# Optimization experiments

Measured on AMD Instinct MI355X. Metric: run time of the kernel, lower is better.

## Reference

```python
import jax, jax.numpy as jnp
import numpy as np

# Problem constants (would come from parameter_group in the original module)
N_POS = 512      # number of scan positions
BATCH = 32       # diffraction patterns per batch
N_OPR = 4        # OPR (orthogonal probe relaxation) modes
N_MODES = 8      # incoherent probe modes
H_OBJ = W_OBJ = 1024
HP = WP = 256    # probe / patch size
N_SLICES = 4     # multislice object
WAVELENGTH = 1.24e-10   # m (10 keV X-rays)
PIXEL = 1.0e-8          # m object pixel size
DZ = 2.0e-6             # m slice spacing


def _as_complex(x):
    return jax.lax.complex(x[..., 0], x[..., 1])


def _angular_spectrum_tf():
    # Transfer function H(fx,fy) = exp(i*dz*kz), kz = 2*pi/lambda * sqrt(1-(l*fx)^2-(l*fy)^2)
    fy = np.fft.fftfreq(HP, d=PIXEL)
    fx = np.fft.fftfreq(WP, d=PIXEL)
    FY, FX = np.meshgrid(fy, fx, indexing='ij')
    arg = 1.0 - (WAVELENGTH * FX) ** 2 - (WAVELENGTH * FY) ** 2
    kz = 2.0 * np.pi / WAVELENGTH * np.sqrt(np.maximum(arg, 0.0))
    tf = np.exp(1j * DZ * kz) * (arg > 0)  # evanescent cutoff
    return jnp.asarray(tf, jnp.complex64)

_TF = _angular_spectrum_tf()


def setup_inputs() -> dict:
    key = jax.random.key(0)
    k1, k2, k3, k4, k5 = jax.random.split(key, 5)
    object_ri = jax.random.normal(k1, (N_SLICES, H_OBJ, W_OBJ, 2), jnp.float32) * 0.1
    # make object roughly a weak phase/amplitude modulator around 1
    object_ri = object_ri.at[..., 0].add(1.0)
    probe_ri = jax.random.normal(k2, (N_OPR, N_MODES, HP, WP, 2), jnp.float32)
    opr_weights = jax.random.normal(k3, (N_POS, N_OPR), jnp.float32) * 0.1
    opr_weights = opr_weights.at[:, 0].add(1.0)
    # positions (row, col) such that the 256x256 patch fits inside the object
    positions = jax.random.uniform(k4, (N_POS, 2), jnp.float32,
                                   minval=16.0, maxval=float(H_OBJ - HP - 16))
    indices = jax.random.randint(k5, (BATCH,), 0, N_POS, jnp.int32)
    return {"object_ri": object_ri, "probe_ri": probe_ri,
            "opr_weights": opr_weights, "positions": positions, "indices": indices}


def reference(object_ri, probe_ri, opr_weights, positions, indices):
    obj = _as_complex(object_ri)      # (S, H, W)
    probe = _as_complex(probe_ri)     # (K, M, h, w)
    pos = positions[indices]          # (B, 2)
    rpos = jnp.round(pos)
    frac = pos - rpos                 # fractional shifts compensated on probe
    ipos = rpos.astype(jnp.int32)

    # --- gather object patches at rounded positions: (B, S, h, w) ---
    def get_patch(rc):
        return jax.lax.dynamic_slice(obj, (0, rc[0], rc[1]), (N_SLICES, HP, WP))
    patches = jax.vmap(get_patch)(ipos)

    # --- unique probes via OPR weighting of mode 0 ---
    w = opr_weights[indices].astype(probe.dtype)           # (B, K)
    p0 = jnp.einsum('bk,khw->bhw', w, probe[:, 0])         # (B, h, w)
    pk = jnp.broadcast_to(probe[0, 1:], (pos.shape[0], N_MODES - 1, HP, WP))
    uprobe = jnp.concatenate([p0[:, None], pk], axis=1)    # (B, M, h, w)

    # --- subpixel Fourier shift of probes by fractional positions ---
    fy = jnp.fft.fftfreq(HP).astype(jnp.float32)
    fx = jnp.fft.fftfreq(WP).astype(jnp.float32)
    ramp = frac[:, 0, None, None] * fy[:, None] + frac[:, 1, None, None] * fx[None, :]
    phase = jnp.exp(jax.lax.complex(jnp.zeros_like(ramp), -2.0 * jnp.pi * ramp))  # (B, h, w)
    uprobe = jnp.fft.ifft2(jnp.fft.fft2(uprobe) * phase[:, None])

    # --- multislice propagation through the object ---
    psi = uprobe
    for s in range(N_SLICES):
        psi = patches[:, s, None] * psi                    # modulate
        if s < N_SLICES - 1:
            psi = jnp.fft.ifft2(jnp.fft.fft2(psi) * _TF)   # angular spectrum

    # --- far-field (Fourier) propagation to detector ---
    psi_far = jnp.fft.fftshift(
        jnp.fft.fft2(jnp.fft.ifftshift(psi, axes=(-2, -1)), norm='ortho'),
        axes=(-2, -1))
    # incoherent sum over probe modes -> detector intensities (B, h, w)
    return jnp.sum(jnp.abs(psi_far) ** 2, axis=1)
```

## Files before the change

### kernel.cpp

```cpp
#include <hip/hip_runtime.h>
#include <math.h>

#define HP 256
#define NB 32
#define NM 8
#define NK 4
#define NS 4
#define HOBJ 1024

__device__ __forceinline__ float2 cmul(float2 a, float2 b) {
    return make_float2(fmaf(a.x, b.x, -a.y * b.y), fmaf(a.x, b.y, a.y * b.x));
}

__constant__ float COS16[10] = {1.f, 0.9238795325f, 0.7071067812f, 0.3826834324f, 0.f,
                                -0.3826834324f, -0.7071067812f, -0.9238795325f, -1.f, -0.9238795325f};
__constant__ float SIN16[10] = {0.f, 0.3826834324f, 0.7071067812f, 0.9238795325f, 1.f,
                                0.9238795325f, 0.7071067812f, 0.3826834324f, 0.f, -0.3826834324f};

template <int S>
__device__ __forceinline__ void dft4(float2 a, float2 b, float2 c, float2 d,
                                     float2* o0, float2* o1, float2* o2, float2* o3) {
    float2 apc = make_float2(a.x + c.x, a.y + c.y);
    float2 amc = make_float2(a.x - c.x, a.y - c.y);
    float2 bpd = make_float2(b.x + d.x, b.y + d.y);
    float2 bmd = make_float2(b.x - d.x, b.y - d.y);
    float2 ib = (S < 0) ? make_float2(bmd.y, -bmd.x) : make_float2(-bmd.y, bmd.x);
    *o0 = make_float2(apc.x + bpd.x, apc.y + bpd.y);
    *o1 = make_float2(amc.x + ib.x, amc.y + ib.y);
    *o2 = make_float2(apc.x - bpd.x, apc.y - bpd.y);
    *o3 = make_float2(amc.x - ib.x, amc.y - ib.y);
}

template <int S>
__device__ __forceinline__ void fft16(float2 v[16]) {
    float2 t[16];
#pragma unroll
    for (int b = 0; b < 4; ++b)
        dft4<S>(v[b], v[4 + b], v[8 + b], v[12 + b],
                &t[4 * b + 0], &t[4 * b + 1], &t[4 * b + 2], &t[4 * b + 3]);
#pragma unroll
    for (int b = 1; b < 4; ++b)
#pragma unroll
        for (int c = 1; c < 4; ++c) {
            int j = b * c;
            float2 w = make_float2(COS16[j], (S < 0) ? -SIN16[j] : SIN16[j]);
            t[4 * b + c] = cmul(t[4 * b + c], w);
        }
#pragma unroll
    for (int c = 0; c < 4; ++c)
        dft4<S>(t[c], t[4 + c], t[8 + c], t[12 + c],
                &v[c + 0], &v[c + 4], &v[c + 8], &v[c + 12]);
}

template <int S, bool BS>
__device__ __forceinline__ void fft256(float2 v[16], int t, float* ldsRe, float* ldsIm) {
    fft16<S>(v);
    float sn, cs;
    __sincosf((float)S * 0.0245436926f  * (float)t, &sn, &cs);
    float2 base = make_float2(cs, sn);
    float2 cur = base;
#pragma unroll
    for (int k = 1; k < 16; ++k) {
        v[k] = cmul(v[k], cur);
        cur = cmul(cur, base);
    }
    if constexpr (BS) __syncthreads(); else asm volatile("" ::: "memory");
#pragma unroll
    for (int k = 0; k < 16; ++k) {
        ldsRe[k * 17 + t] = v[k].x;
        ldsIm[k * 17 + t] = v[k].y;
    }
    if constexpr (BS) __syncthreads(); else asm volatile("" ::: "memory");
#pragma unroll
    for (int j = 0; j < 16; ++j) {
        v[j].x = ldsRe[t * 17 + j];
        v[j].y = ldsIm[t * 17 + j];
    }
    fft16<S>(v);
}

#define ROWSTRIDE 272
#define COLSTRIDE 290

__global__ void k_init_shared(const float* __restrict__ probe, float2* __restrict__ sharedK) {
    __shared__ float sRe[16 * ROWSTRIDE], sIm[16 * ROWSTRIDE];
    int tt = threadIdx.x;
    int t = tt & 15, g = tt >> 4;
    int rowg = blockIdx.x, m = blockIdx.y + 1;
    int y = rowg * 16 + g;
    const float2* p = (const float2*)probe + (size_t)m * 65536 + (size_t)y * 256;
    float2 v[16];
#pragma unroll
    for (int n1 = 0; n1 < 16; ++n1) v[n1] = p[n1 * 16 + t];
    fft256<-1, false>(v, t, &sRe[g * ROWSTRIDE], &sIm[g * ROWSTRIDE]);
    float2* ob = sharedK + (size_t)(m - 1) * 65536 + (size_t)y * 256;
#pragma unroll
    for (int k2 = 0; k2 < 16; ++k2) ob[k2 * 16 + t] = v[k2];
}

__global__ void k_init_m0(const float* __restrict__ probe, const float* __restrict__ opr_w,
                          const int* __restrict__ indices, float2* __restrict__ buf, int b0) {
    __shared__ float sRe[16 * ROWSTRIDE], sIm[16 * ROWSTRIDE];
    int tt = threadIdx.x;
    int t = tt & 15, g = tt >> 4;
    int rowg = blockIdx.x, bl = blockIdx.z;
    int b = b0 + bl;
    int y = rowg * 16 + g;
    int idx = indices[b];
    float w0 = opr_w[idx * 4 + 0], w1 = opr_w[idx * 4 + 1];
    float w2 = opr_w[idx * 4 + 2], w3 = opr_w[idx * 4 + 3];
    const float2* p = (const float2*)probe;
    size_t rb = (size_t)y * 256;
    float2 v[16];
#pragma unroll
    for (int n1 = 0; n1 < 16; ++n1) {
        size_t o = rb + n1 * 16 + t;
        float2 p0 = p[o];
        float2 p1 = p[(size_t)(1 * NM) * 65536 + o];
        float2 p2 = p[(size_t)(2 * NM) * 65536 + o];
        float2 p3 = p[(size_t)(3 * NM) * 65536 + o];
        v[n1] = make_float2(w0 * p0.x + w1 * p1.x + w2 * p2.x + w3 * p3.x,
                            w0 * p0.y + w1 * p1.y + w2 * p2.y + w3 * p3.y);
    }
    fft256<-1, false>(v, t, &sRe[g * ROWSTRIDE], &sIm[g * ROWSTRIDE]);
    float2* ob = buf + (size_t)(bl * NM) * 65536 + (size_t)y * 256;
#pragma unroll
    for (int k2 = 0; k2 < 16; ++k2) ob[k2 * 16 + t] = v[k2];
}

__global__ void k_col_shift(const float* __restrict__ positions, const int* __restrict__ indices,
                            const float2* __restrict__ sharedK, float2* __restrict__ buf, int b0) {
    __shared__ float sRe[16 * COLSTRIDE], sIm[16 * COLSTRIDE];
    int tt = threadIdx.x;
    int c = tt & 15, t = tt >> 4;
    int colg = blockIdx.x, m = blockIdx.y, bl = blockIdx.z;
    int b = b0 + bl;
    int x = colg * 16 + c;
    int idx = indices[b];
    float py = positions[idx * 2 + 0], px = positions[idx * 2 + 1];
    float fr0 = py - rintf(py), fr1 = px - rintf(px);
    const float2* src = m ? (sharedK + (size_t)(m - 1) * 65536)
                          : (buf + (size_t)(bl * NM) * 65536);
    float2* dst = buf + (size_t)(bl * NM + m) * 65536;
    float2 v[16];
#pragma unroll
    for (int n1 = 0; n1 < 16; ++n1) v[n1] = src[(size_t)(n1 * 16 + t) * 256 + x];
    fft256<-1, true>(v, t, &sRe[c * COLSTRIDE], &sIm[c * COLSTRIDE]);
    float fxv = (float)((x < 128) ? x : x - 256) * (1.0f / 256.0f);
    float fy0 = (float)t * (1.0f / 256.0f);
    float sn, cs;
    __sincosf(-6.2831853071795864769f * (fr0 * fy0 + fr1 * fxv), &sn, &cs);
    float2 cur = make_float2(cs, sn);
    __sincosf(-6.2831853071795864769f * fr0 * (1.0f / 16.0f), &sn, &cs);
    float2 step = make_float2(cs, sn);
    __sincosf(6.2831853071795864769f * fr0, &sn, &cs);
    float2 wrap = make_float2(cs, sn);
#pragma unroll
    for (int k2 = 0; k2 < 16; ++k2) {
        if (k2 == 8) cur = cmul(cur, wrap);
        v[k2] = cmul(v[k2], cur);
        cur = cmul(cur, step);
    }
    fft256<1, true>(v, t, &sRe[c * COLSTRIDE], &sIm[c * COLSTRIDE]);
#pragma unroll
    for (int j = 0; j < 16; ++j) {
        float2 r = make_float2(v[j].x * (1.0f / 256.0f), v[j].y * (1.0f / 256.0f));
        dst[(size_t)(j * 16 + t) * 256 + x] = r;
    }
}

__global__ void k_row_prop(const float* __restrict__ object, const float* __restrict__ positions,
                           const int* __restrict__ indices, float2* __restrict__ buf, int b0, int s) {
    __shared__ float sRe[16 * ROWSTRIDE], sIm[16 * ROWSTRIDE];
    int tt = threadIdx.x;
    int t = tt & 15, g = tt >> 4;
    int rowg = blockIdx.x, m = blockIdx.y, bl = blockIdx.z;
    int b = b0 + bl;
    int y = rowg * 16 + g;
    int idx = indices[b];
    int r0 = (int)rintf(positions[idx * 2 + 0]);
    int r1 = (int)rintf(positions[idx * 2 + 1]);
    float2* img = buf + (size_t)(bl * NM + m) * 65536 + (size_t)y * 256;
    float2 v[16];
#pragma unroll
    for (int n1 = 0; n1 < 16; ++n1) v[n1] = img[n1 * 16 + t];
    fft256<1, false>(v, t, &sRe[g * ROWSTRIDE], &sIm[g * ROWSTRIDE]);
    const float2* obj = (const float2*)object + (size_t)s * HOBJ * HOBJ + (size_t)(r0 + y) * HOBJ + r1;
#pragma unroll
    for (int j = 0; j < 16; ++j) {
        int xx = t + 16 * j;
        float2 pz = obj[xx];
        float2 ps = make_float2(v[j].x * (1.0f / 256.0f), v[j].y * (1.0f / 256.0f));
        v[j] = cmul(ps, pz);
    }
    fft256<-1, false>(v, t, &sRe[g * ROWSTRIDE], &sIm[g * ROWSTRIDE]);
#pragma unroll
    for (int k2 = 0; k2 < 16; ++k2) img[k2 * 16 + t] = v[k2];
}

__global__ void k_col_tf(const float2* __restrict__ tf, float2* __restrict__ buf) {
    __shared__ float sRe[16 * COLSTRIDE], sIm[16 * COLSTRIDE];
    int tt = threadIdx.x;
    int c = tt & 15, t = tt >> 4;
    int colg = blockIdx.x, m = blockIdx.y, bl = blockIdx.z;
    int x = colg * 16 + c;
    float2* img = buf + (size_t)(bl * NM + m) * 65536;
    float2 v[16];
#pragma unroll
    for (int n1 = 0; n1 < 16; ++n1) v[n1] = img[(size_t)(n1 * 16 + t) * 256 + x];
    fft256<-1, true>(v, t, &sRe[c * COLSTRIDE], &sIm[c * COLSTRIDE]);
#pragma unroll
    for (int k2 = 0; k2 < 16; ++k2) {
        int ky = t + 16 * k2;
        v[k2] = cmul(v[k2], tf[ky * 256 + x]);
    }
    fft256<1, true>(v, t, &sRe[c * COLSTRIDE], &sIm[c * COLSTRIDE]);
#pragma unroll
    for (int j = 0; j < 16; ++j) {
        float2 r = make_float2(v[j].x * (1.0f / 256.0f), v[j].y * (1.0f / 256.0f));
        img[(size_t)(j * 16 + t) * 256 + x] = r;
    }
}

__global__ void k_col_final(const float2* __restrict__ buf, float* __restrict__ out, int b0) {
    __shared__ float sRe[16 * COLSTRIDE], sIm[16 * COLSTRIDE];
    int tt = threadIdx.x;
    int c = tt & 15, t = tt >> 4;
    int colg = blockIdx.x, bl = blockIdx.z;
    int x = colg * 16 + c;
    float acc[16];
#pragma unroll
    for (int j = 0; j < 16; ++j) acc[j] = 0.f;
    for (int m = 0; m < NM; ++m) {
        const float2* img = buf + (size_t)(bl * NM + m) * 65536;
        float2 v[16];
#pragma unroll
        for (int n1 = 0; n1 < 16; ++n1) v[n1] = img[(size_t)(n1 * 16 + t) * 256 + x];
        fft256<-1, true>(v, t, &sRe[c * COLSTRIDE], &sIm[c * COLSTRIDE]);
#pragma unroll
        for (int k2 = 0; k2 < 16; ++k2)
            acc[k2] = fmaf(v[k2].x, v[k2].x, fmaf(v[k2].y, v[k2].y, acc[k2]));
    }
    int b = b0 + bl;
    float* ob = out + (size_t)b * 65536;
    int xs = (x + 128) & 255;
#pragma unroll
    for (int k2 = 0; k2 < 16; ++k2) {
        int ky = t + 16 * k2;
        int ys = (ky + 128) & 255;
        ob[ys * 256 + xs] = acc[k2] * (1.0f / 65536.0f);
    }
}

__global__ void k_tf(float2* __restrict__ tf) {
    int i = blockIdx.x * 256 + threadIdx.x;
    int ky = i >> 8, kx = i & 255;
    double fy = (double)((ky < 128) ? ky : ky - 256) / (256.0 * 1.0e-8);
    double fx = (double)((kx < 128) ? kx : kx - 256) / (256.0 * 1.0e-8);
    double ly = 1.24e-10 * fy, lx = 1.24e-10 * fx;
    double arg = 1.0 - lx * lx - ly * ly;
    float2 r = make_float2(0.f, 0.f);
    if (arg > 0.0) {
        double kz = (2.0 * M_PI / 1.24e-10) * sqrt(arg);
        double ph = 2.0e-6 * kz;
        r = make_float2((float)cos(ph), (float)sin(ph));
    }
    tf[i] = r;
}

extern "C" void kernel_launch(void* const* d_in, const int* in_sizes, int n_in,
                              void* d_out, int out_size, void* d_ws, size_t ws_size,
                              hipStream_t stream) {
    const float* object = (const float*)d_in[0];
    const float* probe = (const float*)d_in[1];
    const float* opr_w = (const float*)d_in[2];
    const float* positions = (const float*)d_in[3];
    const int* indices = (const int*)d_in[4];
    float* out = (float*)d_out;

    float2* tf = (float2*)d_ws;
    float2* sharedK = (float2*)((char*)d_ws + ((size_t)1 << 20));
    float2* buf = (float2*)((char*)d_ws + ((size_t)8 << 20));
    size_t head = (size_t)8 << 20;
    size_t avail = (ws_size > head) ? ws_size - head : 0;
    long long perb = (long long)NM * 65536 * sizeof(float2);
    int Bc = (int)(avail / perb);
    if (Bc > NB) Bc = NB;
    if (Bc < 1) Bc = 1;

    k_tf<<<256, 256, 0, stream>>>(tf);
    k_init_shared<<<dim3(16, NM - 1, 1), 256, 0, stream>>>(probe, sharedK);

    for (int b0 = 0; b0 < NB; b0 += Bc) {
        int bc = (NB - b0 < Bc) ? (NB - b0) : Bc;
        dim3 grid(16, NM, bc);
        k_init_m0<<<dim3(16, 1, bc), 256, 0, stream>>>(probe, opr_w, indices, buf, b0);
        k_col_shift<<<grid, 256, 0, stream>>>(positions, indices, sharedK, buf, b0);
        for (int s = 0; s < NS; ++s) {
            k_row_prop<<<grid, 256, 0, stream>>>(object, positions, indices, buf, b0, s);
            if (s < NS - 1) k_col_tf<<<grid, 256, 0, stream>>>(tf, buf);
        }
        dim3 gridE(16, 1, bc);
        k_col_final<<<gridE, 256, 0, stream>>>(buf, out, b0);
    }
}
```

Before: 486.7 us.

## Store wavefield buffer in fp16, halve row-FFT LDS, split final mode reduction

Intermediate wavefields between FFT passes are now stored as half2 instead of float2. This halves global memory traffic for the bandwidth-bound multislice row and column passes. Row FFTs transpose real and imaginary parts through a single LDS array, halving shared memory per block to improve occupancy. The final column pass splits the 8 modes across two blocks that write partial sums, and a new add kernel combines them for more parallelism. The fp16 storage trades accuracy (about 11-bit mantissa, limited range) for bandwidth and risks tolerance failures.

```diff
diff --git a/kernel.cpp b/kernel.cpp
--- a/kernel.cpp
+++ b/kernel.cpp
@@ -1,4 +1,5 @@
 #include <hip/hip_runtime.h>
+#include <hip/hip_fp16.h>
 #include <math.h>
 
 #define HP 256
@@ -10,6 +11,13 @@
 
 __device__ __forceinline__ float2 cmul(float2 a, float2 b) {
     return make_float2(fmaf(a.x, b.x, -a.y * b.y), fmaf(a.x, b.y, a.y * b.x));
+}
+
+__device__ __forceinline__ float2 h2f(__half2 h) {
+    return make_float2(__low2float(h), __high2float(h));
+}
+__device__ __forceinline__ __half2 f2h(float2 v) {
+    return __floats2half2_rn(v.x, v.y);
 }
 
 __constant__ float COS16[10] = {1.f, 0.9238795325f, 0.7071067812f, 0.3826834324f, 0.f,
@@ -52,25 +60,54 @@
                 &v[c + 0], &v[c + 4], &v[c + 8], &v[c + 12]);
 }
 
-template <int S, bool BS>
-__device__ __forceinline__ void fft256(float2 v[16], int t, float* ldsRe, float* ldsIm) {
-    fft16<S>(v);
+__device__ __forceinline__ float2 twiddle_base(int S, int t) {
     float sn, cs;
     __sincosf((float)S * 0.0245436926f  * (float)t, &sn, &cs);
-    float2 base = make_float2(cs, sn);
+    return make_float2(cs, sn);
+}
+
+template <int S>
+__device__ __forceinline__ void fft256_w(float2 v[16], int t, float* lds) {
+    fft16<S>(v);
+    float2 base = twiddle_base(S, t);
     float2 cur = base;
 #pragma unroll
     for (int k = 1; k < 16; ++k) {
         v[k] = cmul(v[k], cur);
         cur = cmul(cur, base);
     }
-    if constexpr (BS) __syncthreads(); else asm volatile("" ::: "memory");
+    asm volatile("" ::: "memory");
+#pragma unroll
+    for (int k = 0; k < 16; ++k) lds[k * 17 + t] = v[k].x;
+    asm volatile("" ::: "memory");
+#pragma unroll
+    for (int j = 0; j < 16; ++j) v[j].x = lds[t * 17 + j];
+    asm volatile("" ::: "memory");
+#pragma unroll
+    for (int k = 0; k < 16; ++k) lds[k * 17 + t] = v[k].y;
+    asm volatile("" ::: "memory");
+#pragma unroll
+    for (int j = 0; j < 16; ++j) v[j].y = lds[t * 17 + j];
+    fft16<S>(v);
+}
+
+template <int S>
+__device__ __forceinline__ void fft256_b(float2 v[16], int t, float* ldsRe, float* ldsIm) {
+    fft16<S>(v);
+    float2 base = twiddle_base(S, t);
+    float2 cur = base;
+#pragma unroll
+    for (int k = 1; k < 16; ++k) {
+        v[k] = cmul(v[k], cur);
+        cur = cmul(cur, base);
+    }
+    __syncthreads();
 #pragma unroll
     for (int k = 0; k < 16; ++k) {
         ldsRe[k * 17 + t] = v[k].x;
         ldsIm[k * 17 + t] = v[k].y;
     }
-    if constexpr (BS) __syncthreads(); else asm volatile("" ::: "memory");
+    __syncthreads();
 #pragma unroll
     for (int j = 0; j < 16; ++j) {
         v[j].x = ldsRe[t * 17 + j];
@@ -83,7 +120,7 @@
 #define COLSTRIDE 290
 
 __global__ void k_init_shared(const float* __restrict__ probe, float2* __restrict__ sharedK) {
-    __shared__ float sRe[16 * ROWSTRIDE], sIm[16 * ROWSTRIDE];
+    __shared__ float sc[16 * ROWSTRIDE];
     int tt = threadIdx.x;
     int t = tt & 15, g = tt >> 4;
     int rowg = blockIdx.x, m = blockIdx.y + 1;
@@ -92,15 +129,15 @@
     float2 v[16];
 #pragma unroll
     for (int n1 = 0; n1 < 16; ++n1) v[n1] = p[n1 * 16 + t];
-    fft256<-1, false>(v, t, &sRe[g * ROWSTRIDE], &sIm[g * ROWSTRIDE]);
+    fft256_w<-1>(v, t, &sc[g * ROWSTRIDE]);
     float2* ob = sharedK + (size_t)(m - 1) * 65536 + (size_t)y * 256;
 #pragma unroll
     for (int k2 = 0; k2 < 16; ++k2) ob[k2 * 16 + t] = v[k2];
 }
 
 __global__ void k_init_m0(const float* __restrict__ probe, const float* __restrict__ opr_w,
-                          const int* __restrict__ indices, float2* __restrict__ buf, int b0) {
-    __shared__ float sRe[16 * ROWSTRIDE], sIm[16 * ROWSTRIDE];
+                          const int* __restrict__ indices, __half2* __restrict__ buf, int b0) {
+    __shared__ float sc[16 * ROWSTRIDE];
     int tt = threadIdx.x;
     int t = tt & 15, g = tt >> 4;
     int rowg = blockIdx.x, bl = blockIdx.z;
@@ -122,14 +159,14 @@
         v[n1] = make_float2(w0 * p0.x + w1 * p1.x + w2 * p2.x + w3 * p3.x,
                             w0 * p0.y + w1 * p1.y + w2 * p2.y + w3 * p3.y);
     }
-    fft256<-1, false>(v, t, &sRe[g * ROWSTRIDE], &sIm[g * ROWSTRIDE]);
-    float2* ob = buf + (size_t)(bl * NM) * 65536 + (size_t)y * 256;
-#pragma unroll
-    for (int k2 = 0; k2 < 16; ++k2) ob[k2 * 16 + t] = v[k2];
+    fft256_w<-1>(v, t, &sc[g * ROWSTRIDE]);
+    __half2* ob = buf + (size_t)(bl * NM) * 65536 + (size_t)y * 256;
+#pragma unroll
+    for (int k2 = 0; k2 < 16; ++k2) ob[k2 * 16 + t] = f2h(v[k2]);
 }
 
 __global__ void k_col_shift(const float* __restrict__ positions, const int* __restrict__ indices,
-                            const float2* __restrict__ sharedK, float2* __restrict__ buf, int b0) {
+                            const float2* __restrict__ sharedK, __half2* __restrict__ buf, int b0) {
     __shared__ float sRe[16 * COLSTRIDE], sIm[16 * COLSTRIDE];
     int tt = threadIdx.x;
     int c = tt & 15, t = tt >> 4;
@@ -139,13 +176,18 @@
     int idx = indices[b];
     float py = positions[idx * 2 + 0], px = positions[idx * 2 + 1];
     float fr0 = py - rintf(py), fr1 = px - rintf(px);
-    const float2* src = m ? (sharedK + (size_t)(m - 1) * 65536)
-                          : (buf + (size_t)(bl * NM) * 65536);
-    float2* dst = buf + (size_t)(bl * NM + m) * 65536;
-    float2 v[16];
-#pragma unroll
-    for (int n1 = 0; n1 < 16; ++n1) v[n1] = src[(size_t)(n1 * 16 + t) * 256 + x];
-    fft256<-1, true>(v, t, &sRe[c * COLSTRIDE], &sIm[c * COLSTRIDE]);
+    float2 v[16];
+    if (m) {
+        const float2* src = sharedK + (size_t)(m - 1) * 65536;
+#pragma unroll
+        for (int n1 = 0; n1 < 16; ++n1) v[n1] = src[(size_t)(n1 * 16 + t) * 256 + x];
+    } else {
+        const __half2* src = buf + (size_t)(bl * NM) * 65536;
+#pragma unroll
+        for (int n1 = 0; n1 < 16; ++n1) v[n1] = h2f(src[(size_t)(n1 * 16 + t) * 256 + x]);
+    }
+    __half2* dst = buf + (size_t)(bl * NM + m) * 65536;
+    fft256_b<-1>(v, t, &sRe[c * COLSTRIDE], &sIm[c * COLSTRIDE]);
     float fxv = (float)((x < 128) ? x : x - 256) * (1.0f / 256.0f);
     float fy0 = (float)t * (1.0f / 256.0f);
     float sn, cs;
@@ -161,17 +203,17 @@
         v[k2] = cmul(v[k2], cur);
         cur = cmul(cur, step);
     }
-    fft256<1, true>(v, t, &sRe[c * COLSTRIDE], &sIm[c * COLSTRIDE]);
+    fft256_b<1>(v, t, &sRe[c * COLSTRIDE], &sIm[c * COLSTRIDE]);
 #pragma unroll
     for (int j = 0; j < 16; ++j) {
         float2 r = make_float2(v[j].x * (1.0f / 256.0f), v[j].y * (1.0f / 256.0f));
-        dst[(size_t)(j * 16 + t) * 256 + x] = r;
+        dst[(size_t)(j * 16 + t) * 256 + x] = f2h(r);
     }
 }
 
 __global__ void k_row_prop(const float* __restrict__ object, const float* __restrict__ positions,
-                           const int* __restrict__ indices, float2* __restrict__ buf, int b0, int s) {
-    __shared__ float sRe[16 * ROWSTRIDE], sIm[16 * ROWSTRIDE];
+                           const int* __restrict__ indices, __half2* __restrict__ buf, int b0, int s) {
+    __shared__ float sc[16 * ROWSTRIDE];
     int tt = threadIdx.x;
     int t = tt & 15, g = tt >> 4;
     int rowg = blockIdx.x, m = blockIdx.y, bl = blockIdx.z;
@@ -180,11 +222,11 @@
     int idx = indices[b];
     int r0 = (int)rintf(positions[idx * 2 + 0]);
     int r1 = (int)rintf(positions[idx * 2 + 1]);
-    float2* img = buf + (size_t)(bl * NM + m) * 65536 + (size_t)y * 256;
-    float2 v[16];
-#pragma unroll
-    for (int n1 = 0; n1 < 16; ++n1) v[n1] = img[n1 * 16 + t];
-    fft256<1, false>(v, t, &sRe[g * ROWSTRIDE], &sIm[g * ROWSTRIDE]);
+    __half2* img = buf + (size_t)(bl * NM + m) * 65536 + (size_t)y * 256;
+    float2 v[16];
+#pragma unroll
+    for (int n1 = 0; n1 < 16; ++n1) v[n1] = h2f(img[n1 * 16 + t]);
+    fft256_w<1>(v, t, &sc[g * ROWSTRIDE]);
     const float2* obj = (const float2*)object + (size_t)s * HOBJ * HOBJ + (size_t)(r0 + y) * HOBJ + r1;
 #pragma unroll
     for (int j = 0; j < 16; ++j) {
@@ -193,56 +235,59 @@
         float2 ps = make_float2(v[j].x * (1.0f / 256.0f), v[j].y * (1.0f / 256.0f));
         v[j] = cmul(ps, pz);
     }
-    fft256<-1, false>(v, t, &sRe[g * ROWSTRIDE], &sIm[g * ROWSTRIDE]);
-#pragma unroll
-    for (int k2 = 0; k2 < 16; ++k2) img[k2 * 16 + t] = v[k2];
-}
-
-__global__ void k_col_tf(const float2* __restrict__ tf, float2* __restrict__ buf) {
+    fft256_w<-1>(v, t, &sc[g * ROWSTRIDE]);
+#pragma unroll
+    for (int k2 = 0; k2 < 16; ++k2) img[k2 * 16 + t] = f2h(v[k2]);
+}
+
+__global__ void k_col_tf(const float2* __restrict__ tf, __half2* __restrict__ buf) {
     __shared__ float sRe[16 * COLSTRIDE], sIm[16 * COLSTRIDE];
     int tt = threadIdx.x;
     int c = tt & 15, t = tt >> 4;
     int colg = blockIdx.x, m = blockIdx.y, bl = blockIdx.z;
     int x = colg * 16 + c;
-    float2* img = buf + (size_t)(bl * NM + m) * 65536;
-    float2 v[16];
-#pragma unroll
-    for (int n1 = 0; n1 < 16; ++n1) v[n1] = img[(size_t)(n1 * 16 + t) * 256 + x];
-    fft256<-1, true>(v, t, &sRe[c * COLSTRIDE], &sIm[c * COLSTRIDE]);
+    __half2* img = buf + (size_t)(bl * NM + m) * 65536;
+    float2 v[16];
+#pragma unroll
+    for (int n1 = 0; n1 < 16; ++n1) v[n1] = h2f(img[(size_t)(n1 * 16 + t) * 256 + x]);
+    fft256_b<-1>(v, t, &sRe[c * COLSTRIDE], &sIm[c * COLSTRIDE]);
 #pragma unroll
     for (int k2 = 0; k2 < 16; ++k2) {
         int ky = t + 16 * k2;
         v[k2] = cmul(v[k2], tf[ky * 256 + x]);
     }
-    fft256<1, true>(v, t, &sRe[c * COLSTRIDE], &sIm[c * COLSTRIDE]);
+    fft256_b<1>(v, t, &sRe[c * COLSTRIDE], &sIm[c * COLSTRIDE]);
 #pragma unroll
     for (int j = 0; j < 16; ++j) {
         float2 r = make_float2(v[j].x * (1.0f / 256.0f), v[j].y * (1.0f / 256.0f));
-        img[(size_t)(j * 16 + t) * 256 + x] = r;
-    }
-}
-
-__global__ void k_col_final(const float2* __restrict__ buf, float* __restrict__ out, int b0) {
+        img[(size_t)(j * 16 + t) * 256 + x] = f2h(r);
+    }
+}
+
+__global__ void k_col_final(const __half2* __restrict__ buf, float* __restrict__ out,
+                            float* __restrict__ part, int b0) {
     __shared__ float sRe[16 * COLSTRIDE], sIm[16 * COLSTRIDE];
     int tt = threadIdx.x;
     int c = tt & 15, t = tt >> 4;
-    int colg = blockIdx.x, bl = blockIdx.z;
+    int colg = blockIdx.x, mp = blockIdx.y, bl = blockIdx.z;
     int x = colg * 16 + c;
     float acc[16];
 #pragma unroll
     for (int j = 0; j < 16; ++j) acc[j] = 0.f;
-    for (int m = 0; m < NM; ++m) {
-        const float2* img = buf + (size_t)(bl * NM + m) * 65536;
+#pragma unroll
+    for (int mi = 0; mi < 4; ++mi) {
+        int m = mp * 4 + mi;
+        const __half2* img = buf + (size_t)(bl * NM + m) * 65536;
         float2 v[16];
 #pragma unroll
-        for (int n1 = 0; n1 < 16; ++n1) v[n1] = img[(size_t)(n1 * 16 + t) * 256 + x];
-        fft256<-1, true>(v, t, &sRe[c * COLSTRIDE], &sIm[c * COLSTRIDE]);
+        for (int n1 = 0; n1 < 16; ++n1) v[n1] = h2f(img[(size_t)(n1 * 16 + t) * 256 + x]);
+        fft256_b<-1>(v, t, &sRe[c * COLSTRIDE], &sIm[c * COLSTRIDE]);
 #pragma unroll
         for (int k2 = 0; k2 < 16; ++k2)
             acc[k2] = fmaf(v[k2].x, v[k2].x, fmaf(v[k2].y, v[k2].y, acc[k2]));
     }
     int b = b0 + bl;
-    float* ob = out + (size_t)b * 65536;
+    float* ob = (mp ? part : out) + (size_t)b * 65536;
     int xs = (x + 128) & 255;
 #pragma unroll
     for (int k2 = 0; k2 < 16; ++k2) {
@@ -250,6 +295,13 @@
         int ys = (ky + 128) & 255;
         ob[ys * 256 + xs] = acc[k2] * (1.0f / 65536.0f);
     }
+}
+
+__global__ void k_addout(float* __restrict__ out, const float* __restrict__ part) {
+    int i = blockIdx.x * 256 + threadIdx.x;
+    float4 a = ((const float4*)out)[i];
+    float4 p = ((const float4*)part)[i];
+    ((float4*)out)[i] = make_float4(a.x + p.x, a.y + p.y, a.z + p.z, a.w + p.w);
 }
 
 __global__ void k_tf(float2* __restrict__ tf) {
@@ -280,10 +332,11 @@
 
     float2* tf = (float2*)d_ws;
     float2* sharedK = (float2*)((char*)d_ws + ((size_t)1 << 20));
-    float2* buf = (float2*)((char*)d_ws + ((size_t)8 << 20));
-    size_t head = (size_t)8 << 20;
+    float* part = (float*)((char*)d_ws + ((size_t)8 << 20));
+    __half2* buf = (__half2*)((char*)d_ws + ((size_t)16 << 20));
+    size_t head = (size_t)16 << 20;
     size_t avail = (ws_size > head) ? ws_size - head : 0;
-    long long perb = (long long)NM * 65536 * sizeof(float2);
+    long long perb = (long long)NM * 65536 * sizeof(__half2);
     int Bc = (int)(avail / perb);
     if (Bc > NB) Bc = NB;
     if (Bc < 1) Bc = 1;
@@ -300,7 +353,8 @@
             k_row_prop<<<grid, 256, 0, stream>>>(object, positions, indices, buf, b0, s);
             if (s < NS - 1) k_col_tf<<<grid, 256, 0, stream>>>(tf, buf);
         }
-        dim3 gridE(16, 1, bc);
-        k_col_final<<<gridE, 256, 0, stream>>>(buf, out, b0);
-    }
-}
+        dim3 gridE(16, 2, bc);
+        k_col_final<<<gridE, 256, 0, stream>>>(buf, out, part, b0);
+    }
+    k_addout<<<(NB * 65536) / (256 * 4), 256, 0, stream>>>(out, part);
+}
```

Result: faster. 401.0 us (median of 2 runs) (-17.6%).
